# Kernel tuning notes

Hardware: AMD Instinct MI355X
Metric: run time of the kernel (lower is better)

Reference implementation:

```python
import jax, jax.numpy as jnp
import numpy as np
jax.config.update("jax_enable_x64", True)  # circuit computes internally in FP64

N = 4_194_304  # batch of scalar tanh evaluations
_SHIFTS = jnp.arange(31, -1, -1, dtype=jnp.uint32)  # MSB-first bit order, per make_fp64_constant


def f32_to_bits(v):
    """float32 [...,] -> [..., 32] 0/1 float32 pulses, MSB first."""
    u = jax.lax.bitcast_convert_type(v.astype(jnp.float32), jnp.uint32)
    return ((u[..., None] >> _SHIFTS) & jnp.uint32(1)).astype(jnp.float32)


def bits_to_f32(bits):
    """[..., 32] 0/1 pulses (MSB first) -> float32 [...]."""
    u = jnp.sum(bits.astype(jnp.uint32) << _SHIFTS, axis=-1, dtype=jnp.uint32)
    return jax.lax.bitcast_convert_type(u, jnp.float32)


def setup_inputs() -> dict:
    key = jax.random.key(0)
    vals = (jax.random.normal(key, (N,), dtype=jnp.float32) * 2.0).astype(jnp.float32)
    x = f32_to_bits(vals)  # [N, 32] valid IEEE-754 bit pulses
    return {"x": x}


def reference(x) -> jnp.ndarray:
    # The SNN circuit: FP32 bits -> FP64, then tanh(v) = (e^{2v} - 1) / (e^{2v} + 1)
    # entirely in FP64 arithmetic, then round back to FP32 bits.
    v64 = bits_to_f32(x).astype(jnp.float64)          # FP32ToFP64Converter
    e2x = jnp.exp(jnp.float64(2.0) * v64)             # fp64_mul + fp64_exp
    t64 = (e2x - 1.0) / (e2x + 1.0)                   # fp64_adder x2 + fp64_divider
    return f32_to_bits(t64.astype(jnp.float32))       # FP64ToFP32Converter -> [N, 32] pulses
```

## Files before the change

### kernel.cpp

```cpp
#include <hip/hip_runtime.h>

typedef unsigned int uint32;
typedef unsigned int v4u __attribute__((ext_vector_type(4)));

__device__ __forceinline__ uint32 nib_of(v4u b) {
    return ((b.x >> 26) & 8u) | ((b.y >> 27) & 4u) |
           ((b.z >> 28) & 2u) | ((b.w >> 29) & 1u);
}

__device__ __forceinline__ uint32 butterfly_or(uint32 u) {
    u |= __shfl_xor(u, 1);
    u |= __shfl_xor(u, 2);
    u |= __shfl_xor(u, 4);
    return u;
}

__device__ __forceinline__ uint32 tanh_bits(uint32 u) {
    double v = (double)__uint_as_float(u);
    double e2x = exp(2.0 * v);
    double t64 = (e2x - 1.0) / (e2x + 1.0);
    return __float_as_uint((float)t64);
}

__device__ __forceinline__ v4u expand_nibble(uint32 ru, int shift) {
    uint32 onib = (ru >> shift) & 0xFu;
    v4u o;
    o.x = (onib & 8u) ? 0x3F800000u : 0u;
    o.y = (onib & 4u) ? 0x3F800000u : 0u;
    o.z = (onib & 2u) ? 0x3F800000u : 0u;
    o.w = (onib & 1u) ? 0x3F800000u : 0u;
    return o;
}

__global__ __launch_bounds__(256) void
spike_tanh_kernel(const v4u* __restrict__ in, v4u* __restrict__ out,
                  int n_vec4, int n_main) {
    const int stride = gridDim.x * blockDim.x;
    const int shift  = 4 * (7 - (threadIdx.x & 7));
    int i = blockIdx.x * blockDim.x + threadIdx.x;

    for (; i < n_main; i += 4 * stride) {
        v4u a0 = in[i];
        v4u a1 = in[i + stride];
        v4u a2 = in[i + 2 * stride];
        v4u a3 = in[i + 3 * stride];

        uint32 u0 = butterfly_or(nib_of(a0) << shift);
        uint32 u1 = butterfly_or(nib_of(a1) << shift);
        uint32 u2 = butterfly_or(nib_of(a2) << shift);
        uint32 u3 = butterfly_or(nib_of(a3) << shift);

        uint32 r0 = tanh_bits(u0);
        uint32 r1 = tanh_bits(u1);
        uint32 r2 = tanh_bits(u2);
        uint32 r3 = tanh_bits(u3);

        __builtin_nontemporal_store(expand_nibble(r0, shift), out + i);
        __builtin_nontemporal_store(expand_nibble(r1, shift), out + i + stride);
        __builtin_nontemporal_store(expand_nibble(r2, shift), out + i + 2 * stride);
        __builtin_nontemporal_store(expand_nibble(r3, shift), out + i + 3 * stride);
    }
    for (; i < n_vec4; i += stride) {
        v4u a = in[i];
        uint32 r = tanh_bits(butterfly_or(nib_of(a) << shift));
        __builtin_nontemporal_store(expand_nibble(r, shift), out + i);
    }
}

extern "C" void kernel_launch(void* const* d_in, const int* in_sizes, int n_in,
                              void* d_out, int out_size, void* d_ws, size_t ws_size,
                              hipStream_t stream) {
    (void)n_in; (void)d_ws; (void)ws_size; (void)out_size;
    const int n_vec4 = in_sizes[0] / 4;
    const v4u* in  = (const v4u*)d_in[0];
    v4u*       out = (v4u*)d_out;

    const int block = 256;
    long grid_l = ((long)n_vec4 + block - 1) / block;
    int grid = grid_l > 2048 ? 2048 : (int)grid_l;
    const int stride = grid * block;
    const int chunk  = 4 * stride;
    const int n_main = (n_vec4 / chunk) * chunk;
    spike_tanh_kernel<<<grid, block, 0, stream>>>(in, out, n_vec4, n_main);
}
```

Measured before the change: 905.0 us.

## Assemble float bits with wave ballots instead of shuffle butterflies

Replaces the three-step shuffle-xor OR reduction with four wave-wide ballots, one per vector component. Each lane then extracts its 8-lane group's byte, bit-reverses it and interleaves the four bytes to rebuild the 32-bit float. It also switches input loads to nontemporal and cuts the per-iteration unroll from 4 to 2. The goal is fewer cross-lane shuffle instructions, at the cost of extra bit manipulation and less memory-level parallelism per thread.

```diff
diff --git a/kernel.cpp b/kernel.cpp
--- a/kernel.cpp
+++ b/kernel.cpp
@@ -1,18 +1,30 @@
 #include <hip/hip_runtime.h>
 
 typedef unsigned int uint32;
+typedef unsigned long long uint64;
 typedef unsigned int v4u __attribute__((ext_vector_type(4)));
 
-__device__ __forceinline__ uint32 nib_of(v4u b) {
-    return ((b.x >> 26) & 8u) | ((b.y >> 27) & 4u) |
-           ((b.z >> 28) & 2u) | ((b.w >> 29) & 1u);
+__device__ __forceinline__ uint32 spread4(uint32 t) {
+    t = (t | (t << 12)) & 0x000F000Fu;
+    t = (t | (t << 6))  & 0x03030303u;
+    t = (t | (t << 3))  & 0x11111111u;
+    return t;
 }
 
-__device__ __forceinline__ uint32 butterfly_or(uint32 u) {
-    u |= __shfl_xor(u, 1);
-    u |= __shfl_xor(u, 2);
-    u |= __shfl_xor(u, 4);
-    return u;
+__device__ __forceinline__ uint32 brev8(uint32 b) {
+    return __brev(b) >> 24;
+}
+
+__device__ __forceinline__ uint32 assemble_ballot(v4u b, uint32 sh8) {
+    uint64 Bx = __ballot(b.x != 0u);
+    uint64 By = __ballot(b.y != 0u);
+    uint64 Bz = __ballot(b.z != 0u);
+    uint64 Bw = __ballot(b.w != 0u);
+    uint32 rx = brev8((uint32)(Bx >> sh8) & 0xFFu);
+    uint32 ry = brev8((uint32)(By >> sh8) & 0xFFu);
+    uint32 rz = brev8((uint32)(Bz >> sh8) & 0xFFu);
+    uint32 rw = brev8((uint32)(Bw >> sh8) & 0xFFu);
+    return (spread4(rx) << 3) | (spread4(ry) << 2) | (spread4(rz) << 1) | spread4(rw);
 }
 
 __device__ __forceinline__ uint32 tanh_bits(uint32 u) {
@@ -36,33 +48,28 @@
 spike_tanh_kernel(const v4u* __restrict__ in, v4u* __restrict__ out,
                   int n_vec4, int n_main) {
     const int stride = gridDim.x * blockDim.x;
-    const int shift  = 4 * (7 - (threadIdx.x & 7));
+    const int lane   = threadIdx.x & 63;
+    const uint32 sh8 = (uint32)(lane & ~7);
+    const int shift  = 4 * (7 - (lane & 7));
     int i = blockIdx.x * blockDim.x + threadIdx.x;
 
-    for (; i < n_main; i += 4 * stride) {
-        v4u a0 = in[i];
-        v4u a1 = in[i + stride];
-        v4u a2 = in[i + 2 * stride];
-        v4u a3 = in[i + 3 * stride];
+    for (; i < n_main; i += 2 * stride) {
+        const int i1 = i + stride;
+        v4u a0 = __builtin_nontemporal_load(in + i);
+        v4u a1 = __builtin_nontemporal_load(in + i1);
 
-        uint32 u0 = butterfly_or(nib_of(a0) << shift);
-        uint32 u1 = butterfly_or(nib_of(a1) << shift);
-        uint32 u2 = butterfly_or(nib_of(a2) << shift);
-        uint32 u3 = butterfly_or(nib_of(a3) << shift);
+        uint32 u0 = assemble_ballot(a0, sh8);
+        uint32 u1 = assemble_ballot(a1, sh8);
 
         uint32 r0 = tanh_bits(u0);
         uint32 r1 = tanh_bits(u1);
-        uint32 r2 = tanh_bits(u2);
-        uint32 r3 = tanh_bits(u3);
 
         __builtin_nontemporal_store(expand_nibble(r0, shift), out + i);
-        __builtin_nontemporal_store(expand_nibble(r1, shift), out + i + stride);
-        __builtin_nontemporal_store(expand_nibble(r2, shift), out + i + 2 * stride);
-        __builtin_nontemporal_store(expand_nibble(r3, shift), out + i + 3 * stride);
+        __builtin_nontemporal_store(expand_nibble(r1, shift), out + i1);
     }
     for (; i < n_vec4; i += stride) {
-        v4u a = in[i];
-        uint32 r = tanh_bits(butterfly_or(nib_of(a) << shift));
+        v4u a = __builtin_nontemporal_load(in + i);
+        uint32 r = tanh_bits(assemble_ballot(a, sh8));
         __builtin_nontemporal_store(expand_nibble(r, shift), out + i);
     }
 }
@@ -79,7 +86,7 @@
     long grid_l = ((long)n_vec4 + block - 1) / block;
     int grid = grid_l > 2048 ? 2048 : (int)grid_l;
     const int stride = grid * block;
-    const int chunk  = 4 * stride;
+    const int chunk  = 2 * stride;
     const int n_main = (n_vec4 / chunk) * chunk;
     spike_tanh_kernel<<<grid, block, 0, stream>>>(in, out, n_vec4, n_main);
 }
```

New measurement: 866.0 us. -4.3%, faster.

## Deduplicate FP64 tanh across the 8 lanes that share each value

Applied to the files above, without the earlier changes.

Previously all 8 lanes that together hold one value's 32 bit pulses computed the same FP64 exp and divide, so the work was done eight times over. Now each lane in a group of 8 loads 8 strided chunks and picks a different value to evaluate. It computes tanh once, then redistributes the results with __shfl before expanding the output nibbles. The unroll factor doubles to 8, and loads become nontemporal. This adds selects, shuffles and register pressure but removes redundant FP64 math, which likely dominates.

```diff
diff --git a/kernel.cpp b/kernel.cpp
--- a/kernel.cpp
+++ b/kernel.cpp
@@ -35,33 +35,52 @@
 __global__ __launch_bounds__(256) void
 spike_tanh_kernel(const v4u* __restrict__ in, v4u* __restrict__ out,
                   int n_vec4, int n_main) {
-    const int stride = gridDim.x * blockDim.x;
-    const int shift  = 4 * (7 - (threadIdx.x & 7));
+    const int stride  = gridDim.x * blockDim.x;
+    const int lane    = threadIdx.x & 63;
+    const int p       = lane & 7;
+    const int shift   = 4 * (7 - p);
+    const int srcbase = lane & ~7;
     int i = blockIdx.x * blockDim.x + threadIdx.x;
 
-    for (; i < n_main; i += 4 * stride) {
-        v4u a0 = in[i];
-        v4u a1 = in[i + stride];
-        v4u a2 = in[i + 2 * stride];
-        v4u a3 = in[i + 3 * stride];
+    for (; i < n_main; i += 8 * stride) {
+        v4u a0 = __builtin_nontemporal_load(in + i);
+        v4u a1 = __builtin_nontemporal_load(in + i + stride);
+        v4u a2 = __builtin_nontemporal_load(in + i + 2 * stride);
+        v4u a3 = __builtin_nontemporal_load(in + i + 3 * stride);
+        v4u a4 = __builtin_nontemporal_load(in + i + 4 * stride);
+        v4u a5 = __builtin_nontemporal_load(in + i + 5 * stride);
+        v4u a6 = __builtin_nontemporal_load(in + i + 6 * stride);
+        v4u a7 = __builtin_nontemporal_load(in + i + 7 * stride);
 
         uint32 u0 = butterfly_or(nib_of(a0) << shift);
         uint32 u1 = butterfly_or(nib_of(a1) << shift);
         uint32 u2 = butterfly_or(nib_of(a2) << shift);
         uint32 u3 = butterfly_or(nib_of(a3) << shift);
+        uint32 u4 = butterfly_or(nib_of(a4) << shift);
+        uint32 u5 = butterfly_or(nib_of(a5) << shift);
+        uint32 u6 = butterfly_or(nib_of(a6) << shift);
+        uint32 u7 = butterfly_or(nib_of(a7) << shift);
 
-        uint32 r0 = tanh_bits(u0);
-        uint32 r1 = tanh_bits(u1);
-        uint32 r2 = tanh_bits(u2);
-        uint32 r3 = tanh_bits(u3);
+        uint32 U = u0;
+        U = (p == 1) ? u1 : U;
+        U = (p == 2) ? u2 : U;
+        U = (p == 3) ? u3 : U;
+        U = (p == 4) ? u4 : U;
+        U = (p == 5) ? u5 : U;
+        U = (p == 6) ? u6 : U;
+        U = (p == 7) ? u7 : U;
 
-        __builtin_nontemporal_store(expand_nibble(r0, shift), out + i);
-        __builtin_nontemporal_store(expand_nibble(r1, shift), out + i + stride);
-        __builtin_nontemporal_store(expand_nibble(r2, shift), out + i + 2 * stride);
-        __builtin_nontemporal_store(expand_nibble(r3, shift), out + i + 3 * stride);
+        uint32 R = tanh_bits(U);
+
+#pragma unroll
+        for (int k = 0; k < 8; ++k) {
+            uint32 rk = __shfl(R, srcbase + k);
+            __builtin_nontemporal_store(expand_nibble(rk, shift),
+                                        out + i + k * stride);
+        }
     }
     for (; i < n_vec4; i += stride) {
-        v4u a = in[i];
+        v4u a = __builtin_nontemporal_load(in + i);
         uint32 r = tanh_bits(butterfly_or(nib_of(a) << shift));
         __builtin_nontemporal_store(expand_nibble(r, shift), out + i);
     }
@@ -79,7 +98,7 @@
     long grid_l = ((long)n_vec4 + block - 1) / block;
     int grid = grid_l > 2048 ? 2048 : (int)grid_l;
     const int stride = grid * block;
-    const int chunk  = 4 * stride;
+    const int chunk  = 8 * stride;
     const int n_main = (n_vec4 / chunk) * chunk;
     spike_tanh_kernel<<<grid, block, 0, stream>>>(in, out, n_vec4, n_main);
 }
```

Measured after the change: 880.4 us. -2.7%, faster.
